# Kernel tuning notes

Measured on AMD Instinct MI355X. Metric: run time of the kernel, lower is better.

Reference implementation:

```python
import jax, jax.numpy as jnp
from jax import lax
import numpy as np

B = 32768
N_IN = 8
N_HID = 64
N_CTRL = 2
M_SCEN = (1.0, 1.2)          # scenario parameters for f/g
M_NOM = 1.0
CLF_LAM = 1.0
CBF_LAM = 1.0
P_CLF = 100.0
P_CBF = 50.0
QP_ITERS = 80                # fixed-iteration batched ADMM (OSQP-style) replacing CvxpyLayer
RHO = 1.0
SIGMA = 1e-6
INF = jnp.inf


def setup_inputs() -> dict:
    key = jax.random.key(0)
    ks = jax.random.split(key, 16)
    s = 0.3
    return {
        "x":   jax.random.normal(ks[0], (B, N_IN), jnp.float32),
        "VW1": jax.random.normal(ks[1], (N_HID, N_IN), jnp.float32) * s,
        "Vb1": jax.random.normal(ks[2], (N_HID,), jnp.float32) * s,
        "VW2": jax.random.normal(ks[3], (N_HID, N_HID), jnp.float32) * s,
        "Vb2": jax.random.normal(ks[4], (N_HID,), jnp.float32) * s,
        "HW1": jax.random.normal(ks[5], (N_HID, N_IN), jnp.float32) * s,
        "Hb1": jax.random.normal(ks[6], (N_HID,), jnp.float32) * s,
        "HW2": jax.random.normal(ks[7], (N_HID, N_HID), jnp.float32) * s,
        "Hb2": jax.random.normal(ks[8], (N_HID,), jnp.float32) * s,
        "HW3": jax.random.normal(ks[9], (N_HID, N_HID), jnp.float32) * s,
        "Hb3": jax.random.normal(ks[10], (N_HID,), jnp.float32) * s,
        "HW4": jax.random.normal(ks[11], (1, N_HID), jnp.float32) * s,
        "Hb4": jax.random.normal(ks[12], (1,), jnp.float32) * s,
        "G0":  jax.random.normal(ks[13], (N_IN, N_CTRL), jnp.float32) * s,
        "K":   jax.random.normal(ks[14], (N_IN, N_CTRL), jnp.float32) * s,
    }


def _lyapunov(x, W1, b1, W2, b2):
    t1 = jnp.tanh(x @ W1.T + b1)                                   # [B,H]
    t2 = jnp.tanh(t1 @ W2.T + b2)                                  # [B,H]
    V = 0.5 * jnp.sum(t2 * t2, axis=1)                             # [B]
    # fused diag(1-t^2) @ W chain (no diag_embed materialization)
    D1 = (1.0 - t1 ** 2)[:, :, None] * W1[None]                    # [B,H,N]
    D2 = (1.0 - t2 ** 2)[:, :, None] * jnp.einsum('hk,bkn->bhn', W2, D1)
    grad_V = jnp.einsum('bh,bhn->bn', t2, D2)                      # [B,N]
    return V, grad_V


def _barrier(x, W1, b1, W2, b2, W3, b3, W4, b4):
    t1 = jnp.tanh(x @ W1.T + b1)
    t2 = jnp.tanh(t1 @ W2.T + b2)
    t3 = jnp.tanh(t2 @ W3.T + b3)
    H = t3 @ W4.T + b4                                             # [B,1]
    D1 = (1.0 - t1 ** 2)[:, :, None] * W1[None]
    D2 = (1.0 - t2 ** 2)[:, :, None] * jnp.einsum('hk,bkn->bhn', W2, D1)
    D3 = (1.0 - t3 ** 2)[:, :, None] * jnp.einsum('hk,bkn->bhn', W3, D2)
    grad_H = jnp.einsum('oh,bhn->bn', W4, D3)                      # [B,N] (o=1)
    return H, grad_H


def _solve_qp(q, A, lo, hi):
    """Batched OSQP-style ADMM for min 0.5 z^T P z + q^T z  s.t. lo <= A z <= hi.
    P = diag([2,2,0,0,0,0]); z = [u(2), r_clf(2), s_cbf(2)]. Fixed iterations."""
    nb, mc, nz = A.shape[0], A.shape[1], A.shape[2]
    Pdiag = jnp.array([2.0, 2.0, 0.0, 0.0, 0.0, 0.0], q.dtype)
    M = RHO * jnp.einsum('bmi,bmj->bij', A, A) + jnp.diag(Pdiag + SIGMA)
    Minv = jnp.linalg.inv(M)                                       # [B,6,6]
    x0 = jnp.zeros((nb, nz), q.dtype)
    z0 = jnp.zeros((nb, mc), q.dtype)
    y0 = jnp.zeros((nb, mc), q.dtype)

    def step(carry, _):
        xx, zz, yy = carry
        rhs = SIGMA * xx - q + jnp.einsum('bmi,bm->bi', A, RHO * zz - yy)
        xt = jnp.einsum('bij,bj->bi', Minv, rhs)
        zt = jnp.einsum('bmi,bi->bm', A, xt)
        zn = jnp.clip(zt + yy / RHO, lo, hi)
        yn = yy + RHO * (zt - zn)
        return (xt, zn, yn), None

    (xf, _, _), _ = lax.scan(step, (x0, z0, y0), None, length=QP_ITERS)
    return xf                                                      # [B,6]


def _forward(x, VW1, Vb1, VW2, Vb2, HW1, Hb1, HW2, Hb2, HW3, Hb3, HW4, Hb4, G0, K):
    V, grad_V = _lyapunov(x, VW1, Vb1, VW2, Vb2)
    H, grad_H = _barrier(x, HW1, Hb1, HW2, Hb2, HW3, Hb3, HW4, Hb4)

    LfVs, LgVs, LfHs, LgHs = [], [], [], []
    for m in M_SCEN:
        # f(x,m) = -x/m ; g(x,m) = G0/m
        LfVs.append(-jnp.sum(grad_V * x, axis=1) / m)              # [B]
        LgVs.append((grad_V @ G0) / m)                             # [B,C]
        LfHs.append(-jnp.sum(grad_H * x, axis=1) / m)
        LgHs.append((grad_H @ G0) / m)
    u_nom = -(x @ K) * (1.0 / M_NOM)                               # [B,C]

    nb = x.shape[0]
    z2 = jnp.zeros((nb, 2), x.dtype)
    ey = jnp.eye(2, dtype=x.dtype)
    e = lambda i: jnp.broadcast_to(ey[i], (nb, 2))
    ninf = jnp.full((nb,), -INF, x.dtype)
    pinf = jnp.full((nb,), INF, x.dtype)
    zer = jnp.zeros((nb,), x.dtype)

    rows, los, his = [], [], []
    for i in range(len(M_SCEN)):
        # CBF: LfH + LgH@u + cbf_lam*H + s_i >= 0
        rows.append(jnp.concatenate([LgHs[i], z2, e(i)], axis=1))
        los.append(-(LfHs[i] + CBF_LAM * H[:, 0])); his.append(pinf)
        # CLF: LfV + LgV@u + clf_lam*V - r_i <= 0
        rows.append(jnp.concatenate([LgVs[i], -e(i), z2], axis=1))
        los.append(ninf); his.append(-(LfVs[i] + CLF_LAM * V))
    for i in range(len(M_SCEN)):
        rows.append(jnp.concatenate([z2, e(i), z2], axis=1)); los.append(zer); his.append(pinf)
    for i in range(len(M_SCEN)):
        rows.append(jnp.concatenate([z2, z2, e(i)], axis=1)); los.append(zer); his.append(pinf)

    A = jnp.stack(rows, axis=1)                                    # [B,8,6]
    lo = jnp.stack(los, axis=1)                                    # [B,8]
    hi = jnp.stack(his, axis=1)
    # objective ||u-u_nom||^2 + p_clf*sum r + p_cbf*sum s  ->  q = [-2 u_nom, p_clf, p_clf, p_cbf, p_cbf]
    q = jnp.concatenate([-2.0 * u_nom,
                         jnp.full((nb, 2), P_CLF, x.dtype),
                         jnp.full((nb, 2), P_CBF, x.dtype)], axis=1)

    z = _solve_qp(q, A, lo, hi)                                    # [B,6]
    u = z[:, :N_CTRL]
    relaxation = jnp.mean(z[:, N_CTRL:N_CTRL + len(M_SCEN)], axis=1, keepdims=True)  # [B,1]

    ns = float(len(M_SCEN))
    Vdot = sum(LfVs[i] + jnp.sum(LgVs[i] * u, axis=1) for i in range(len(M_SCEN))) / ns
    Hdot = sum(LfHs[i] + jnp.sum(LgHs[i] * u, axis=1) for i in range(len(M_SCEN))) / ns
    return u, relaxation, V, Vdot[:, None, None], H, Hdot[:, None, None]


def reference(x, VW1, Vb1, VW2, Vb2, HW1, Hb1, HW2, Hb2, HW3, Hb3, HW4, Hb4, G0, K):
    return _forward(x, VW1, Vb1, VW2, Vb2, HW1, Hb1, HW2, Hb2, HW3, Hb3, HW4, Hb4, G0, K)
```

## Files before the change

kernel.cpp:

```cpp
#include <hip/hip_runtime.h>
#include <hip/hip_bf16.h>
#include <math.h>

#define BTOT 32768

typedef _Float16 f16x8 __attribute__((ext_vector_type(8)));
typedef _Float16 f16x4 __attribute__((ext_vector_type(4)));
typedef float    f32x4 __attribute__((ext_vector_type(4)));

__device__ __forceinline__ float ldin(const void* p, int i, int f32f) {
  return f32f ? ((const float*)p)[i]
              : __bfloat162float(((const __hip_bfloat16*)p)[i]);
}

__device__ __forceinline__ f32x4 MFMA(f16x8 a, f16x8 b, f32x4 c) {
  return __builtin_amdgcn_mfma_f32_16x16x32_f16(a, b, c, 0, 0, 0);
}

__device__ __forceinline__ float tanh_fast(float x) {
  float e = __expf(2.f * x);
  return 1.f - 2.f * __builtin_amdgcn_rcpf(e + 1.f);
}

__device__ __forceinline__ float redq(float v) {
  v += __shfl_xor(v, 16, 64);
  v += __shfl_xor(v, 32, 64);
  return v;
}

__device__ __forceinline__ int widx(int h, int k) {
  return ((h >> 4) << 10) + ((k >> 5) << 9) + (((k >> 3) & 3) << 7) + ((h & 15) << 3) + (k & 7);
}

#define OFF_VW2   0
#define OFF_VW2T  4096
#define OFF_HW2   8192
#define OFF_HW2T  12288
#define OFF_HW3   16384
#define OFF_HW3T  20480
#define OFF_W1VH  24576
#define OFF_W1VL  25088
#define OFF_W1HH  25600
#define OFF_W1HL  26112
#define CF_BASE   28672
#define C_WGV0 0
#define C_WGV1 64
#define C_WGH0 128
#define C_WGH1 192
#define C_VB1  256
#define C_VB2  320
#define C_HB1  384
#define C_HB2  448
#define C_HB3  512
#define C_W4   576
#define C_K    640
#define C_HB4  656
#define C_FLAG 657
#define C_N    658

__global__ __launch_bounds__(256) void prep_kernel(
    const void* px, const void* pVW1, const void* pVW2,
    const void* pHW1, const void* pHW2, const void* pHW3,
    const void* pVb1, const void* pVb2, const void* pHb1, const void* pHb2,
    const void* pHb3, const void* pHW4, const void* pHb4,
    const void* pG0, const void* pK, _Float16* wsp)
{
  __shared__ int sCnt;
  const int tid = threadIdx.x;
  if (tid == 0) sCnt = 0;
  __syncthreads();
  {
    const unsigned short* xb = (const unsigned short*)px;
    int good = 0;
#pragma unroll
    for (int i = 0; i < 2; ++i) {
      int ex = (xb[tid * 2 + i] >> 7) & 0xFF;
      good += (ex >= 97 && ex <= 157) ? 1 : 0;
    }
    atomicAdd(&sCnt, good);
  }
  __syncthreads();
  const int f32f = (sCnt >= 435) ? 0 : 1;

  const int t = blockIdx.x * 256 + tid;
  int h = t >> 6, k = t & 63;
  int fw = widx(h, k), tw = widx(k, h);
  _Float16 v;
  v = (_Float16)ldin(pVW2, t, f32f); wsp[OFF_VW2 + fw] = v; wsp[OFF_VW2T + tw] = v;
  v = (_Float16)ldin(pHW2, t, f32f); wsp[OFF_HW2 + fw] = v; wsp[OFF_HW2T + tw] = v;
  v = (_Float16)ldin(pHW3, t, f32f); wsp[OFF_HW3 + fw] = v; wsp[OFF_HW3T + tw] = v;
  if (t < 512) {
    float f = ldin(pVW1, t, f32f); _Float16 hh = (_Float16)f;
    wsp[OFF_W1VH + t] = hh; wsp[OFF_W1VL + t] = (_Float16)(f - (float)hh);
    f = ldin(pHW1, t, f32f); hh = (_Float16)f;
    wsp[OFF_W1HH + t] = hh; wsp[OFF_W1HL + t] = (_Float16)(f - (float)hh);
  }
  if (blockIdx.x == 0) {
    float* wsF = (float*)(wsp + CF_BASE);
    if (tid < 64) {
      float a0 = 0.f, a1 = 0.f, b0 = 0.f, b1 = 0.f;
#pragma unroll
      for (int nn = 0; nn < 8; ++nn) {
        float g0 = ldin(pG0, 2 * nn, f32f), g1 = ldin(pG0, 2 * nn + 1, f32f);
        float wv = ldin(pVW1, tid * 8 + nn, f32f), wh = ldin(pHW1, tid * 8 + nn, f32f);
        a0 += wv * g0; a1 += wv * g1; b0 += wh * g0; b1 += wh * g1;
      }
      wsF[C_WGV0 + tid] = a0; wsF[C_WGV1 + tid] = a1;
      wsF[C_WGH0 + tid] = b0; wsF[C_WGH1 + tid] = b1;
      wsF[C_VB1 + tid] = ldin(pVb1, tid, f32f);
      wsF[C_VB2 + tid] = ldin(pVb2, tid, f32f);
      wsF[C_HB1 + tid] = ldin(pHb1, tid, f32f);
      wsF[C_HB2 + tid] = ldin(pHb2, tid, f32f);
      wsF[C_HB3 + tid] = ldin(pHb3, tid, f32f);
      wsF[C_W4  + tid] = ldin(pHW4, tid, f32f);
    }
    if (tid < 16) wsF[C_K + tid] = ldin(pK, tid, f32f);
    if (tid == 0) { wsF[C_HB4] = ldin(pHb4, 0, f32f); ((int*)wsF)[C_FLAG] = f32f; }
  }
}

__global__ __launch_bounds__(512, 4) void main_kernel(
    const void* px, const _Float16* wsp, float* out)
{
  __shared__ __align__(16) _Float16 sAct[4][4][1024];
  __shared__ __align__(16) float sQPp[8][16][12];
  __shared__ __align__(16) float sC[C_N];

  const int tid = threadIdx.x, lane = tid & 63, wave = tid >> 6;
  const int pair = wave >> 1, sub = wave & 1;
  const int m = lane & 15, q = lane >> 4;
  const int ro = lane * 8;
  const int e0 = blockIdx.x * 64 + pair * 16;

  const float* wsF = (const float*)(wsp + CF_BASE);
  for (int i = tid; i < C_N; i += 512) sC[i] = wsF[i];
  const int f32f = ((const int*)wsF)[C_FLAG];
  const bool wsplit = (f32f != 0);

  f16x8 zf;
#pragma unroll
  for (int i = 0; i < 8; ++i) zf[i] = (_Float16)0.f;

  f16x8 xbh = zf, xbl = zf;
  if (lane < 16) {
#pragma unroll
    for (int n = 0; n < 8; ++n) {
      float v = ldin(px, (e0 + m) * 8 + n, f32f);
      _Float16 hh = (_Float16)v;
      xbh[n] = hh; xbl[n] = (_Float16)(v - (float)hh);
    }
  }
  __syncthreads();

  if (sub == 0 && lane < 16) {
    float un0 = 0.f, un1 = 0.f;
#pragma unroll
    for (int n = 0; n < 8; ++n) {
      float xv = (float)xbh[n] + (float)xbl[n];
      un0 -= xv * sC[C_K + 2 * n];
      un1 -= xv * sC[C_K + 2 * n + 1];
    }
    sQPp[wave][m][8] = un0; sQPp[wave][m][9] = un1;
  }

  _Float16* bufV0 = sAct[pair][0];
  _Float16* bufV1 = sAct[pair][1];
  _Float16* bufH0 = sAct[pair][2];
  _Float16* bufH1 = sAct[pair][3];

  auto hgemm = [&](int poff, const _Float16* a_, f32x4* acc) {
    f16x8 b0 = *(const f16x8*)(a_ + ro);
    f16x8 b1 = *(const f16x8*)(a_ + 512 + ro);
#pragma unroll
    for (int i = 0; i < 2; ++i) {
      const _Float16* ap = wsp + poff + (2 * sub + i) * 1024 + ro;
      f32x4 c = {0.f, 0.f, 0.f, 0.f};
      c = MFMA(*(const f16x8*)ap, b0, c);
      c = MFMA(*(const f16x8*)(ap + 512), b1, c);
      acc[i] = c;
    }
  };
  auto wstore = [&](const f32x4* vals, _Float16* a_) {
#pragma unroll
    for (int i = 0; i < 2; ++i) {
      int ht = 2 * sub + i;
      int aw = ((ht >> 1) << 9) + (((ht & 1) * 2 + (q >> 1)) << 7) + m * 8 + ((q & 1) << 2);
      f16x4 vh;
#pragma unroll
      for (int r = 0; r < 4; ++r) vh[r] = (_Float16)vals[i][r];
      *(f16x4*)(a_ + aw) = vh;
    }
  };
  auto l1gemm = [&](int hoff, int loff, f32x4* acc) {
#pragma unroll
    for (int i = 0; i < 2; ++i) {
      int ht = 2 * sub + i;
      f16x8 afh = zf, afl = zf;
      if (lane < 16) {
        afh = *(const f16x8*)(wsp + hoff + (ht * 16 + m) * 8);
        afl = *(const f16x8*)(wsp + loff + (ht * 16 + m) * 8);
      }
      f32x4 c = {0.f, 0.f, 0.f, 0.f};
      c = MFMA(afh, xbh, c);
      c = MFMA(afh, xbl, c);
      if (wsplit) c = MFMA(afl, xbh, c);
      acc[i] = c;
    }
  };

  f32x4 accV[2], accH[2], z1V[2], z1H[2], d1V[2], d1H[2], d2H[2], tvV[2], tvH[2];

  l1gemm(OFF_W1VH, OFF_W1VL, accV);
  l1gemm(OFF_W1HH, OFF_W1HL, accH);
#pragma unroll
  for (int i = 0; i < 2; ++i) {
    int hb = (2 * sub + i) * 16 + q * 4;
    z1V[i] = accV[i]; z1H[i] = accH[i];
    f32x4 bV = *(const f32x4*)&sC[C_VB1 + hb];
    f32x4 bH = *(const f32x4*)&sC[C_HB1 + hb];
#pragma unroll
    for (int r = 0; r < 4; ++r) {
      float t = tanh_fast(z1V[i][r] + bV[r]);
      tvV[i][r] = t; d1V[i][r] = 1.f - t * t;
      t = tanh_fast(z1H[i][r] + bH[r]);
      tvH[i][r] = t; d1H[i][r] = 1.f - t * t;
    }
  }
  wstore(tvV, bufV0); wstore(tvH, bufH0);
  __syncthreads();

  hgemm(OFF_VW2, bufV0, accV);
  hgemm(OFF_HW2, bufH0, accH);
  float pV = 0.f;
#pragma unroll
  for (int i = 0; i < 2; ++i) {
    int hb = (2 * sub + i) * 16 + q * 4;
    f32x4 bV = *(const f32x4*)&sC[C_VB2 + hb];
    f32x4 bH = *(const f32x4*)&sC[C_HB2 + hb];
#pragma unroll
    for (int r = 0; r < 4; ++r) {
      float t = tanh_fast(accV[i][r] + bV[r]);
      pV += t * t;
      tvV[i][r] = t * (1.f - t * t);
      t = tanh_fast(accH[i][r] + bH[r]);
      tvH[i][r] = t; d2H[i][r] = 1.f - t * t;
    }
  }
  wstore(tvV, bufV1); wstore(tvH, bufH1);
  __syncthreads();

  hgemm(OFF_VW2T, bufV1, accV);
  hgemm(OFF_HW3, bufH1, accH);
  float pgvx = 0.f, plv0 = 0.f, plv1 = 0.f, pH = 0.f;
#pragma unroll
  for (int i = 0; i < 2; ++i) {
    int hb = (2 * sub + i) * 16 + q * 4;
    f32x4 g0 = *(const f32x4*)&sC[C_WGV0 + hb];
    f32x4 g1 = *(const f32x4*)&sC[C_WGV1 + hb];
    f32x4 bH = *(const f32x4*)&sC[C_HB3 + hb];
    f32x4 w4 = *(const f32x4*)&sC[C_W4 + hb];
#pragma unroll
    for (int r = 0; r < 4; ++r) {
      float wt = accV[i][r] * d1V[i][r];
      pgvx += wt * z1V[i][r];
      plv0 += wt * g0[r]; plv1 += wt * g1[r];
      float t = tanh_fast(accH[i][r] + bH[r]);
      pH += t * w4[r];
      tvH[i][r] = w4[r] * (1.f - t * t);
    }
  }
  wstore(tvH, bufH0);
  __syncthreads();

  hgemm(OFF_HW3T, bufH0, accH);
#pragma unroll
  for (int i = 0; i < 2; ++i)
#pragma unroll
    for (int r = 0; r < 4; ++r) tvH[i][r] = accH[i][r] * d2H[i][r];
  wstore(tvH, bufH1);
  __syncthreads();

  hgemm(OFF_HW2T, bufH1, accH);
  float pghx = 0.f, plh0 = 0.f, plh1 = 0.f;
#pragma unroll
  for (int i = 0; i < 2; ++i) {
    int hb = (2 * sub + i) * 16 + q * 4;
    f32x4 g0 = *(const f32x4*)&sC[C_WGH0 + hb];
    f32x4 g1 = *(const f32x4*)&sC[C_WGH1 + hb];
#pragma unroll
    for (int r = 0; r < 4; ++r) {
      float wt = accH[i][r] * d1H[i][r];
      pghx += wt * z1H[i][r];
      plh0 += wt * g0[r]; plh1 += wt * g1[r];
    }
  }

  {
    float a0 = redq(plh0), a1 = redq(plh1), a2 = redq(plv0), a3 = redq(plv1);
    float a4 = redq(pghx), a5 = redq(pgvx), a6 = redq(pV), a7 = redq(pH);
    if (lane < 16) {
      sQPp[wave][lane][0] = a0; sQPp[wave][lane][1] = a1;
      sQPp[wave][lane][2] = a2; sQPp[wave][lane][3] = a3;
      sQPp[wave][lane][4] = a4; sQPp[wave][lane][5] = a5;
      sQPp[wave][lane][6] = a6; sQPp[wave][lane][7] = a7;
    }
  }
  __syncthreads();

  if (tid >= 64) return;
  const int p = tid >> 4, mm = tid & 15;
  const int e = blockIdx.x * 64 + tid;
  float gh0 = sQPp[2 * p][mm][0] + sQPp[2 * p + 1][mm][0];
  float gh1 = sQPp[2 * p][mm][1] + sQPp[2 * p + 1][mm][1];
  float gv0 = sQPp[2 * p][mm][2] + sQPp[2 * p + 1][mm][2];
  float gv1 = sQPp[2 * p][mm][3] + sQPp[2 * p + 1][mm][3];
  float ghx = sQPp[2 * p][mm][4] + sQPp[2 * p + 1][mm][4];
  float gvx = sQPp[2 * p][mm][5] + sQPp[2 * p + 1][mm][5];
  float V   = 0.5f * (sQPp[2 * p][mm][6] + sQPp[2 * p + 1][mm][6]);
  float H   = sQPp[2 * p][mm][7] + sQPp[2 * p + 1][mm][7] + sC[C_HB4];
  float un0 = sQPp[2 * p][mm][8], un1 = sQPp[2 * p][mm][9];
  out[98304 + e]  = V;
  out[163840 + e] = H;

  const float im = 1.0f / 1.2f;
  const float sg = 1e-6f;

  float lo0 = ghx - H;
  float hi1 = gvx - V;
  float lo2 = ghx * im - H;
  float hi3 = gvx * im - V;
  float qv0 = -2.f * un0, qv1 = -2.f * un1;

  const float d  = 2.f + sg;
  const float rd = 1.f / d;
  const float al = 1.f + im * im;
  const float be = al * (1.f - rd);
  float S00 = be * (gh0 * gh0 + gv0 * gv0) + d;
  float S11 = be * (gh1 * gh1 + gv1 * gv1) + d;
  float S01 = be * (gh0 * gh1 + gv0 * gv1);
  float idet = 1.f / (S00 * S11 - S01 * S01);
  float i00 = S11 * idet, i11 = S00 * idet, i01 = -S01 * idet;

  float X0 = 0.f, X1 = 0.f, X2 = 0.f, X3 = 0.f, X4 = 0.f, X5 = 0.f;
  float Z[8] = {0.f, 0.f, 0.f, 0.f, 0.f, 0.f, 0.f, 0.f};
  float Y[8] = {0.f, 0.f, 0.f, 0.f, 0.f, 0.f, 0.f, 0.f};

#pragma unroll 1
  for (int it = 0; it < 80; ++it) {
    float t0 = Z[0] - Y[0], t1 = Z[1] - Y[1], t2 = Z[2] - Y[2], t3 = Z[3] - Y[3];
    float t4 = Z[4] - Y[4], t5 = Z[5] - Y[5], t6 = Z[6] - Y[6], t7 = Z[7] - Y[7];
    float tauh = t0 + im * t2, tauv = t1 + im * t3;
    float b0 = sg * X0 - qv0 + gh0 * tauh + gv0 * tauv;
    float b1 = sg * X1 - qv1 + gh1 * tauh + gv1 * tauv;
    float b2 = sg * X2 - 100.f - t1 + t4;
    float b3 = sg * X3 - 100.f - t3 + t5;
    float b4 = sg * X4 - 50.f + t0 + t6;
    float b5 = sg * X5 - 50.f + t2 + t7;
    float pp = b2 + im * b3;
    float s2 = b4 + im * b5;
    float cb0 = gh0 * s2 - gv0 * pp;
    float cb1 = gh1 * s2 - gv1 * pp;
    float u0b = b0 - cb0 * rd;
    float u1b = b1 - cb1 * rd;
    X0 = i00 * u0b + i01 * u1b;
    X1 = i01 * u0b + i11 * u1b;
    float gdH = gh0 * X0 + gh1 * X1;
    float gdV = gv0 * X0 + gv1 * X1;
    X2 = (b2 + gdV) * rd;
    X3 = (b3 + im * gdV) * rd;
    X4 = (b4 - gdH) * rd;
    X5 = (b5 - im * gdH) * rd;
    float zt0 = gdH + X4;
    float zt1 = gdV - X2;
    float zt2 = gdH * im + X5;
    float zt3 = gdV * im - X3;

    float v, zn;
    v = zt0 + Y[0]; zn = fmaxf(v, lo0); Y[0] += zt0 - zn; Z[0] = zn;
    v = zt1 + Y[1]; zn = fminf(v, hi1); Y[1] += zt1 - zn; Z[1] = zn;
    v = zt2 + Y[2]; zn = fmaxf(v, lo2); Y[2] += zt2 - zn; Z[2] = zn;
    v = zt3 + Y[3]; zn = fminf(v, hi3); Y[3] += zt3 - zn; Z[3] = zn;
    v = X2 + Y[4];  zn = fmaxf(v, 0.f); Y[4] += X2 - zn;  Z[4] = zn;
    v = X3 + Y[5];  zn = fmaxf(v, 0.f); Y[5] += X3 - zn;  Z[5] = zn;
    v = X4 + Y[6];  zn = fmaxf(v, 0.f); Y[6] += X4 - zn;  Z[6] = zn;
    v = X5 + Y[7];  zn = fmaxf(v, 0.f); Y[7] += X5 - zn;  Z[7] = zn;
  }

  float relax = 0.5f * (X2 + X3);
  const float cc = 0.5f * (1.f + im);
  float Vdot = cc * (gv0 * X0 + gv1 * X1 - gvx);
  float Hdot = cc * (gh0 * X0 + gh1 * X1 - ghx);

  out[2 * e]      = X0;
  out[2 * e + 1]  = X1;
  out[65536 + e]  = relax;
  out[131072 + e] = Vdot;
  out[196608 + e] = Hdot;
}

extern "C" void kernel_launch(void* const* d_in, const int* in_sizes, int n_in,
                              void* d_out, int out_size, void* d_ws, size_t ws_size,
                              hipStream_t stream) {
  float* out = (float*)d_out;
  _Float16* wsp = (_Float16*)d_ws;
  prep_kernel<<<16, 256, 0, stream>>>(
      d_in[0], d_in[1], d_in[3], d_in[5], d_in[7], d_in[9],
      d_in[2], d_in[4], d_in[6], d_in[8], d_in[10], d_in[11], d_in[12],
      d_in[13], d_in[14], wsp);
  main_kernel<<<512, 512, 0, stream>>>(d_in[0], wsp, out);
}
```

Measured before the change: 110.2 us.

## Split hidden tiles across four waves per group and pack layer-1 hi/lo split into one MFMA

Doubles the block to 1024 threads so each 16-element group is handled by four waves, each owning one 16-row hidden tile instead of two. Layer-1 hi/lo precision splitting is packed into the K dimension of a single 16x16x32 MFMA via a new prepacked weight layout, replacing two or three MFMAs. The aim is shorter per-wave dependency chains and more waves in flight to hide latency. In exchange there are more waves contending at each barrier, a final reduction over four partials, and the low-part correction term is now always applied.

```diff
diff --git a/kernel.cpp b/kernel.cpp
--- a/kernel.cpp
+++ b/kernel.cpp
@@ -30,6 +30,9 @@
 
 __device__ __forceinline__ int widx(int h, int k) {
   return ((h >> 4) << 10) + ((k >> 5) << 9) + (((k >> 3) & 3) << 7) + ((h & 15) << 3) + (k & 7);
+}
+__device__ __forceinline__ int pidx(int h, int k) {
+  return ((h >> 4) << 9) + (((k >> 3) & 3) << 7) + ((h & 15) << 3) + (k & 7);
 }
 
 #define OFF_VW2   0
@@ -38,10 +41,8 @@
 #define OFF_HW2T  12288
 #define OFF_HW3   16384
 #define OFF_HW3T  20480
-#define OFF_W1VH  24576
-#define OFF_W1VL  25088
-#define OFF_W1HH  25600
-#define OFF_W1HL  26112
+#define OFF_W1PV  24576
+#define OFF_W1PH  26624
 #define CF_BASE   28672
 #define C_WGV0 0
 #define C_WGV1 64
@@ -83,17 +84,24 @@
   const int f32f = (sCnt >= 435) ? 0 : 1;
 
   const int t = blockIdx.x * 256 + tid;
-  int h = t >> 6, k = t & 63;
-  int fw = widx(h, k), tw = widx(k, h);
-  _Float16 v;
-  v = (_Float16)ldin(pVW2, t, f32f); wsp[OFF_VW2 + fw] = v; wsp[OFF_VW2T + tw] = v;
-  v = (_Float16)ldin(pHW2, t, f32f); wsp[OFF_HW2 + fw] = v; wsp[OFF_HW2T + tw] = v;
-  v = (_Float16)ldin(pHW3, t, f32f); wsp[OFF_HW3 + fw] = v; wsp[OFF_HW3T + tw] = v;
-  if (t < 512) {
-    float f = ldin(pVW1, t, f32f); _Float16 hh = (_Float16)f;
-    wsp[OFF_W1VH + t] = hh; wsp[OFF_W1VL + t] = (_Float16)(f - (float)hh);
-    f = ldin(pHW1, t, f32f); hh = (_Float16)f;
-    wsp[OFF_W1HH + t] = hh; wsp[OFF_W1HL + t] = (_Float16)(f - (float)hh);
+  {
+    int h = t >> 6, k = t & 63;
+    int fw = widx(h, k), tw = widx(k, h);
+    _Float16 v;
+    v = (_Float16)ldin(pVW2, t, f32f); wsp[OFF_VW2 + fw] = v; wsp[OFF_VW2T + tw] = v;
+    v = (_Float16)ldin(pHW2, t, f32f); wsp[OFF_HW2 + fw] = v; wsp[OFF_HW2T + tw] = v;
+    v = (_Float16)ldin(pHW3, t, f32f); wsp[OFF_HW3 + fw] = v; wsp[OFF_HW3T + tw] = v;
+  }
+  if (t < 2048) {
+    int h = t >> 5, k = t & 31;
+    int j = k & 7, sec = k >> 3;
+    int slot = pidx(h, k);
+    float fv = ldin(pVW1, h * 8 + j, f32f);
+    _Float16 vh = (_Float16)fv, vl = (_Float16)(fv - (float)vh);
+    wsp[OFF_W1PV + slot] = (sec <= 1) ? vh : (sec == 2 ? vl : (_Float16)0.f);
+    fv = ldin(pHW1, h * 8 + j, f32f);
+    vh = (_Float16)fv; vl = (_Float16)(fv - (float)vh);
+    wsp[OFF_W1PH + slot] = (sec <= 1) ? vh : (sec == 2 ? vl : (_Float16)0.f);
   }
   if (blockIdx.x == 0) {
     float* wsF = (float*)(wsp + CF_BASE);
@@ -119,35 +127,36 @@
   }
 }
 
-__global__ __launch_bounds__(512, 4) void main_kernel(
+__global__ __launch_bounds__(1024, 8) void main_kernel(
     const void* px, const _Float16* wsp, float* out)
 {
   __shared__ __align__(16) _Float16 sAct[4][4][1024];
-  __shared__ __align__(16) float sQPp[8][16][12];
+  __shared__ __align__(16) float sQPp[16][16][10];
   __shared__ __align__(16) float sC[C_N];
 
   const int tid = threadIdx.x, lane = tid & 63, wave = tid >> 6;
-  const int pair = wave >> 1, sub = wave & 1;
+  const int pair = wave >> 2, sub = wave & 3;
   const int m = lane & 15, q = lane >> 4;
   const int ro = lane * 8;
   const int e0 = blockIdx.x * 64 + pair * 16;
 
   const float* wsF = (const float*)(wsp + CF_BASE);
-  for (int i = tid; i < C_N; i += 512) sC[i] = wsF[i];
+  for (int i = tid; i < C_N; i += 1024) sC[i] = wsF[i];
   const int f32f = ((const int*)wsF)[C_FLAG];
-  const bool wsplit = (f32f != 0);
 
   f16x8 zf;
 #pragma unroll
   for (int i = 0; i < 8; ++i) zf[i] = (_Float16)0.f;
 
-  f16x8 xbh = zf, xbl = zf;
-  if (lane < 16) {
+  f16x8 xpk = zf;
+  float xf[8];
+  if (q < 3) {
 #pragma unroll
     for (int n = 0; n < 8; ++n) {
       float v = ldin(px, (e0 + m) * 8 + n, f32f);
+      xf[n] = v;
       _Float16 hh = (_Float16)v;
-      xbh[n] = hh; xbl[n] = (_Float16)(v - (float)hh);
+      xpk[n] = (q == 1) ? (_Float16)(v - (float)hh) : hh;
     }
   }
   __syncthreads();
@@ -156,9 +165,8 @@
     float un0 = 0.f, un1 = 0.f;
 #pragma unroll
     for (int n = 0; n < 8; ++n) {
-      float xv = (float)xbh[n] + (float)xbl[n];
-      un0 -= xv * sC[C_K + 2 * n];
-      un1 -= xv * sC[C_K + 2 * n + 1];
+      un0 -= xf[n] * sC[C_K + 2 * n];
+      un1 -= xf[n] * sC[C_K + 2 * n + 1];
     }
     sQPp[wave][m][8] = un0; sQPp[wave][m][9] = un1;
   }
@@ -168,62 +176,44 @@
   _Float16* bufH0 = sAct[pair][2];
   _Float16* bufH1 = sAct[pair][3];
 
-  auto hgemm = [&](int poff, const _Float16* a_, f32x4* acc) {
+  auto hgemm = [&](int poff, const _Float16* a_, f32x4& acc) {
     f16x8 b0 = *(const f16x8*)(a_ + ro);
     f16x8 b1 = *(const f16x8*)(a_ + 512 + ro);
-#pragma unroll
-    for (int i = 0; i < 2; ++i) {
-      const _Float16* ap = wsp + poff + (2 * sub + i) * 1024 + ro;
-      f32x4 c = {0.f, 0.f, 0.f, 0.f};
-      c = MFMA(*(const f16x8*)ap, b0, c);
-      c = MFMA(*(const f16x8*)(ap + 512), b1, c);
-      acc[i] = c;
-    }
+    const _Float16* ap = wsp + poff + sub * 1024 + ro;
+    f32x4 c = {0.f, 0.f, 0.f, 0.f};
+    c = MFMA(*(const f16x8*)ap, b0, c);
+    c = MFMA(*(const f16x8*)(ap + 512), b1, c);
+    acc = c;
   };
-  auto wstore = [&](const f32x4* vals, _Float16* a_) {
-#pragma unroll
-    for (int i = 0; i < 2; ++i) {
-      int ht = 2 * sub + i;
-      int aw = ((ht >> 1) << 9) + (((ht & 1) * 2 + (q >> 1)) << 7) + m * 8 + ((q & 1) << 2);
-      f16x4 vh;
-#pragma unroll
-      for (int r = 0; r < 4; ++r) vh[r] = (_Float16)vals[i][r];
-      *(f16x4*)(a_ + aw) = vh;
-    }
+  auto wstore = [&](const f32x4& vals, _Float16* a_) {
+    int ht = sub;
+    int aw = ((ht >> 1) << 9) + (((ht & 1) * 2 + (q >> 1)) << 7) + m * 8 + ((q & 1) << 2);
+    f16x4 vh;
+#pragma unroll
+    for (int r = 0; r < 4; ++r) vh[r] = (_Float16)vals[r];
+    *(f16x4*)(a_ + aw) = vh;
   };
-  auto l1gemm = [&](int hoff, int loff, f32x4* acc) {
-#pragma unroll
-    for (int i = 0; i < 2; ++i) {
-      int ht = 2 * sub + i;
-      f16x8 afh = zf, afl = zf;
-      if (lane < 16) {
-        afh = *(const f16x8*)(wsp + hoff + (ht * 16 + m) * 8);
-        afl = *(const f16x8*)(wsp + loff + (ht * 16 + m) * 8);
-      }
-      f32x4 c = {0.f, 0.f, 0.f, 0.f};
-      c = MFMA(afh, xbh, c);
-      c = MFMA(afh, xbl, c);
-      if (wsplit) c = MFMA(afl, xbh, c);
-      acc[i] = c;
-    }
+  auto l1gemm = [&](int poff, f32x4& acc) {
+    f16x8 af = *(const f16x8*)(wsp + poff + sub * 512 + lane * 8);
+    f32x4 c = {0.f, 0.f, 0.f, 0.f};
+    acc = MFMA(af, xpk, c);
   };
 
-  f32x4 accV[2], accH[2], z1V[2], z1H[2], d1V[2], d1H[2], d2H[2], tvV[2], tvH[2];
-
-  l1gemm(OFF_W1VH, OFF_W1VL, accV);
-  l1gemm(OFF_W1HH, OFF_W1HL, accH);
-#pragma unroll
-  for (int i = 0; i < 2; ++i) {
-    int hb = (2 * sub + i) * 16 + q * 4;
-    z1V[i] = accV[i]; z1H[i] = accH[i];
+  f32x4 accV, accH, z1V, z1H, d1V, d1H, d2H, tvV, tvH;
+  const int hb = sub * 16 + q * 4;
+
+  l1gemm(OFF_W1PV, accV);
+  l1gemm(OFF_W1PH, accH);
+  {
+    z1V = accV; z1H = accH;
     f32x4 bV = *(const f32x4*)&sC[C_VB1 + hb];
     f32x4 bH = *(const f32x4*)&sC[C_HB1 + hb];
 #pragma unroll
     for (int r = 0; r < 4; ++r) {
-      float t = tanh_fast(z1V[i][r] + bV[r]);
-      tvV[i][r] = t; d1V[i][r] = 1.f - t * t;
-      t = tanh_fast(z1H[i][r] + bH[r]);
-      tvH[i][r] = t; d1H[i][r] = 1.f - t * t;
+      float t = tanh_fast(z1V[r] + bV[r]);
+      tvV[r] = t; d1V[r] = 1.f - t * t;
+      t = tanh_fast(z1H[r] + bH[r]);
+      tvH[r] = t; d1H[r] = 1.f - t * t;
     }
   }
   wstore(tvV, bufV0); wstore(tvH, bufH0);
@@ -232,18 +222,16 @@
   hgemm(OFF_VW2, bufV0, accV);
   hgemm(OFF_HW2, bufH0, accH);
   float pV = 0.f;
-#pragma unroll
-  for (int i = 0; i < 2; ++i) {
-    int hb = (2 * sub + i) * 16 + q * 4;
+  {
     f32x4 bV = *(const f32x4*)&sC[C_VB2 + hb];
     f32x4 bH = *(const f32x4*)&sC[C_HB2 + hb];
 #pragma unroll
     for (int r = 0; r < 4; ++r) {
-      float t = tanh_fast(accV[i][r] + bV[r]);
+      float t = tanh_fast(accV[r] + bV[r]);
       pV += t * t;
-      tvV[i][r] = t * (1.f - t * t);
-      t = tanh_fast(accH[i][r] + bH[r]);
-      tvH[i][r] = t; d2H[i][r] = 1.f - t * t;
+      tvV[r] = t * (1.f - t * t);
+      t = tanh_fast(accH[r] + bH[r]);
+      tvH[r] = t; d2H[r] = 1.f - t * t;
     }
   }
   wstore(tvV, bufV1); wstore(tvH, bufH1);
@@ -252,21 +240,19 @@
   hgemm(OFF_VW2T, bufV1, accV);
   hgemm(OFF_HW3, bufH1, accH);
   float pgvx = 0.f, plv0 = 0.f, plv1 = 0.f, pH = 0.f;
-#pragma unroll
-  for (int i = 0; i < 2; ++i) {
-    int hb = (2 * sub + i) * 16 + q * 4;
+  {
     f32x4 g0 = *(const f32x4*)&sC[C_WGV0 + hb];
     f32x4 g1 = *(const f32x4*)&sC[C_WGV1 + hb];
     f32x4 bH = *(const f32x4*)&sC[C_HB3 + hb];
     f32x4 w4 = *(const f32x4*)&sC[C_W4 + hb];
 #pragma unroll
     for (int r = 0; r < 4; ++r) {
-      float wt = accV[i][r] * d1V[i][r];
-      pgvx += wt * z1V[i][r];
+      float wt = accV[r] * d1V[r];
+      pgvx += wt * z1V[r];
       plv0 += wt * g0[r]; plv1 += wt * g1[r];
-      float t = tanh_fast(accH[i][r] + bH[r]);
+      float t = tanh_fast(accH[r] + bH[r]);
       pH += t * w4[r];
-      tvH[i][r] = w4[r] * (1.f - t * t);
+      tvH[r] = w4[r] * (1.f - t * t);
     }
   }
   wstore(tvH, bufH0);
@@ -274,23 +260,19 @@
 
   hgemm(OFF_HW3T, bufH0, accH);
 #pragma unroll
-  for (int i = 0; i < 2; ++i)
-#pragma unroll
-    for (int r = 0; r < 4; ++r) tvH[i][r] = accH[i][r] * d2H[i][r];
+  for (int r = 0; r < 4; ++r) tvH[r] = accH[r] * d2H[r];
   wstore(tvH, bufH1);
   __syncthreads();
 
   hgemm(OFF_HW2T, bufH1, accH);
   float pghx = 0.f, plh0 = 0.f, plh1 = 0.f;
-#pragma unroll
-  for (int i = 0; i < 2; ++i) {
-    int hb = (2 * sub + i) * 16 + q * 4;
+  {
     f32x4 g0 = *(const f32x4*)&sC[C_WGH0 + hb];
     f32x4 g1 = *(const f32x4*)&sC[C_WGH1 + hb];
 #pragma unroll
     for (int r = 0; r < 4; ++r) {
-      float wt = accH[i][r] * d1H[i][r];
-      pghx += wt * z1H[i][r];
+      float wt = accH[r] * d1H[r];
+      pghx += wt * z1H[r];
       plh0 += wt * g0[r]; plh1 += wt * g1[r];
     }
   }
@@ -310,15 +292,16 @@
   if (tid >= 64) return;
   const int p = tid >> 4, mm = tid & 15;
   const int e = blockIdx.x * 64 + tid;
-  float gh0 = sQPp[2 * p][mm][0] + sQPp[2 * p + 1][mm][0];
-  float gh1 = sQPp[2 * p][mm][1] + sQPp[2 * p + 1][mm][1];
-  float gv0 = sQPp[2 * p][mm][2] + sQPp[2 * p + 1][mm][2];
-  float gv1 = sQPp[2 * p][mm][3] + sQPp[2 * p + 1][mm][3];
-  float ghx = sQPp[2 * p][mm][4] + sQPp[2 * p + 1][mm][4];
-  float gvx = sQPp[2 * p][mm][5] + sQPp[2 * p + 1][mm][5];
-  float V   = 0.5f * (sQPp[2 * p][mm][6] + sQPp[2 * p + 1][mm][6]);
-  float H   = sQPp[2 * p][mm][7] + sQPp[2 * p + 1][mm][7] + sC[C_HB4];
-  float un0 = sQPp[2 * p][mm][8], un1 = sQPp[2 * p][mm][9];
+  float gh0 = 0.f, gh1 = 0.f, gv0 = 0.f, gv1 = 0.f, ghx = 0.f, gvx = 0.f, Vs = 0.f, Hs = 0.f;
+#pragma unroll
+  for (int s = 0; s < 4; ++s) {
+    const float* qp = sQPp[4 * p + s][mm];
+    gh0 += qp[0]; gh1 += qp[1]; gv0 += qp[2]; gv1 += qp[3];
+    ghx += qp[4]; gvx += qp[5]; Vs += qp[6]; Hs += qp[7];
+  }
+  float V = 0.5f * Vs;
+  float H = Hs + sC[C_HB4];
+  float un0 = sQPp[4 * p][mm][8], un1 = sQPp[4 * p][mm][9];
   out[98304 + e]  = V;
   out[163840 + e] = H;
 
@@ -407,5 +390,5 @@
       d_in[0], d_in[1], d_in[3], d_in[5], d_in[7], d_in[9],
       d_in[2], d_in[4], d_in[6], d_in[8], d_in[10], d_in[11], d_in[12],
       d_in[13], d_in[14], wsp);
-  main_kernel<<<512, 512, 0, stream>>>(d_in[0], wsp, out);
-}
+  main_kernel<<<512, 1024, 0, stream>>>(d_in[0], wsp, out);
+}
```

Result: slower. 117.2 us (+6.4%).
